# Kernel tuning notes

Measured on AMD Instinct MI355X. Metric: run time of the kernel, lower is better.

## Reference

```python
import jax, jax.numpy as jnp
import numpy as np

B, N, D, H, W, C = 2, 4, 48, 28, 60, 64
DOWNSAMPLE = 8
NX, NY, NZ = 192, 192, 1   # from size=(192,192), scale=0.25; zbound=[-10,10,20] -> nz=1
SCALE = 0.25
OFFSETX = 0
DMIN, DMAX, DSTEP = 2.0, 50.0, 1.0


def setup_inputs() -> dict:
    key = jax.random.key(0)
    x = jax.random.normal(key, (B, N, D, H, W, C), dtype=jnp.float32)
    ogfW, ogfH = W * DOWNSAMPLE, H * DOWNSAMPLE
    fx = fy = 250.0
    K = jnp.array([[fx, 0.0, ogfW / 2.0], [0.0, fy, ogfH / 2.0], [0.0, 0.0, 1.0]], jnp.float32)
    intrinsics = jnp.broadcast_to(K, (B, N, 3, 3))
    # camera->ego rotation: cam z (forward) -> ego x, cam x (right) -> ego -y, cam y (down) -> ego -z
    R = jnp.array([[0.0, 0.0, 1.0], [-1.0, 0.0, 0.0], [0.0, -1.0, 0.0]], jnp.float32)
    pose = jnp.zeros((B, N, 4, 4), jnp.float32)
    pose = pose.at[..., :3, :3].set(R)
    pose = pose.at[..., :3, 3].set(jnp.array([1.0, 0.0, 1.6], jnp.float32))
    pose = pose.at[..., 3, 3].set(1.0)
    return {"x": x, "intrinsics": intrinsics, "pose": pose}


def _frustum():
    # (D,H,W,3) frustum of (u*d, v*d, d) homogeneous pixel coords scaled by depth
    ds = jnp.arange(DMIN, DMAX, DSTEP, dtype=jnp.float32)          # (D,)
    xs = jnp.linspace(0.0, W * DOWNSAMPLE - 1, W, dtype=jnp.float32)
    ys = jnp.linspace(0.0, H * DOWNSAMPLE - 1, H, dtype=jnp.float32)
    d = jnp.broadcast_to(ds[:, None, None], (D, H, W))
    u = jnp.broadcast_to(xs[None, None, :], (D, H, W))
    v = jnp.broadcast_to(ys[None, :, None], (D, H, W))
    return jnp.stack([u * d, v * d, d], axis=-1)


def reference(x, intrinsics, pose):
    rots = pose[..., :3, :3]                 # (B,N,3,3)
    trans = pose[..., :3, 3]                 # (B,N,3)
    pts = _frustum()                         # (D,H,W,3)
    combine = rots @ jnp.linalg.inv(intrinsics)  # (B,N,3,3)
    # ego-frame point cloud: (B,N,D,H,W,3)
    geom = jnp.einsum('bnij,dhwj->bndhwi', combine, pts) + trans[:, :, None, None, None, :]
    # bev_intrinsics from bev_params_to_intrinsics(size, scale, offsetx)
    f_bev = 1.0 / SCALE
    cx_bev = NX / 2.0 + OFFSETX
    cy_bev = NY / 2.0
    # torch .long() truncates toward zero, same as astype(int32)
    gx = (geom[..., 0] * f_bev + cx_bev).astype(jnp.int32)
    gy = (geom[..., 1] * f_bev + cy_bev).astype(jnp.int32)
    gz = ((geom[..., 2] + 10.0) / 20.0).astype(jnp.int32)  # (z - bx2 + dx2/2)/dx2, bx2=0, dx2=20
    b = jnp.broadcast_to(jnp.arange(B, dtype=jnp.int32)[:, None, None, None, None], gx.shape)
    kept = (gx >= 0) & (gx < NX) & (gy >= 0) & (gy < NY) & (gz >= 0) & (gz < NZ)
    # segment scatter-add == sort + cumsum-diff + scatter-set (ranks unique after reduction)
    flat = ((b * NZ + gz) * NY + gy) * NX + gx
    flat = jnp.where(kept, flat, 0).reshape(-1)
    xf = jnp.where(kept[..., None], x, jnp.zeros((), x.dtype)).reshape(-1, C)
    out = jnp.zeros((B * NZ * NY * NX, C), x.dtype).at[flat].add(xf)
    out = out.reshape(B, NZ, NY, NX, C)
    # final[b, :, z, y, x] layout then cat(unbind(dim=2), dim=1) -> (B, NZ*C, NY, NX)
    return out.transpose(0, 1, 4, 2, 3).reshape(B, NZ * C, NY, NX)
```

## Files before the change

### kernel.cpp

```cpp
#include <hip/hip_runtime.h>

#define BB 2
#define NN 4
#define DD 48
#define HH 28
#define WW 60
#define CC 64
#define NXg 192
#define NYg 192
#define NZg 1
#define DOWNS 8

constexpr int PTS    = BB * NN * DD * HH * WW;
constexpr int NCELLS = BB * NZg * NYg * NXg;
constexpr int CH_STRIDE = NYg * NXg;
constexpr int CHUNK = 64;
constexpr int MAXWORK = NCELLS + PTS / CHUNK + 64;
constexpr int NBLK = NCELLS / 1024;

__global__ void __launch_bounds__(256)
geom_hist_kernel(const float* __restrict__ intr,
                 const float* __restrict__ pose,
                 int* __restrict__ sidx,
                 int* __restrict__ rankv,
                 int* __restrict__ counts) {
    __shared__ int hkey[512];
    __shared__ int hval[512];
    __shared__ int hbase[512];

    int tid = threadIdx.x;
    for (int s = tid; s < 512; s += 256) { hkey[s] = -1; hval[s] = 0; }
    __syncthreads();

    int p = blockIdx.x * blockDim.x + tid;
    int w = p % WW;
    int t = p / WW;
    int h = t % HH; t /= HH;
    int d = t % DD; t /= DD;
    int n = t % NN;
    int b = t / NN;

    const float* K  = intr + (size_t)(b * NN + n) * 9;
    const float* Pm = pose + (size_t)(b * NN + n) * 16;

    double k00 = K[0], k01 = K[1], k02 = K[2];
    double k10 = K[3], k11 = K[4], k12 = K[5];
    double k20 = K[6], k21 = K[7], k22 = K[8];

    double det = k00 * (k11 * k22 - k12 * k21)
               - k01 * (k10 * k22 - k12 * k20)
               + k02 * (k10 * k21 - k11 * k20);
    double id = 1.0 / det;
    double i00 = (k11 * k22 - k12 * k21) * id;
    double i01 = (k02 * k21 - k01 * k22) * id;
    double i02 = (k01 * k12 - k02 * k11) * id;
    double i10 = (k12 * k20 - k10 * k22) * id;
    double i11 = (k00 * k22 - k02 * k20) * id;
    double i12 = (k02 * k10 - k00 * k12) * id;
    double i20 = (k10 * k21 - k11 * k20) * id;
    double i21 = (k01 * k20 - k00 * k21) * id;
    double i22 = (k00 * k11 - k01 * k10) * id;

    double r00 = Pm[0],  r01 = Pm[1],  r02 = Pm[2],  tx = Pm[3];
    double r10 = Pm[4],  r11 = Pm[5],  r12 = Pm[6],  ty = Pm[7];
    double r20 = Pm[8],  r21 = Pm[9],  r22 = Pm[10], tz = Pm[11];

    double c00 = r00 * i00 + r01 * i10 + r02 * i20;
    double c01 = r00 * i01 + r01 * i11 + r02 * i21;
    double c02 = r00 * i02 + r01 * i12 + r02 * i22;
    double c10 = r10 * i00 + r11 * i10 + r12 * i20;
    double c11 = r10 * i01 + r11 * i11 + r12 * i21;
    double c12 = r10 * i02 + r11 * i12 + r12 * i22;
    double c20 = r20 * i00 + r21 * i10 + r22 * i20;
    double c21 = r20 * i01 + r21 * i11 + r22 * i21;
    double c22 = r20 * i02 + r21 * i12 + r22 * i22;

    double u   = (double)w * ((double)(WW * DOWNS - 1) / (double)(WW - 1));
    double v   = (double)h * ((double)(HH * DOWNS - 1) / (double)(HH - 1));
    double dep = 2.0 + (double)d;
    double px = u * dep, py = v * dep, pz = dep;

    double gxf = (c00 * px + c01 * py + c02 * pz + tx) * 4.0 + 96.0;
    double gyf = (c10 * px + c11 * py + c12 * pz + ty) * 4.0 + 96.0;
    double gzf = ((c20 * px + c21 * py + c22 * pz + tz) + 10.0) / 20.0;

    int gx = (int)gxf;
    int gy = (int)gyf;
    int gz = (int)gzf;

    bool kept = (gx >= 0) & (gx < NXg) & (gy >= 0) & (gy < NYg) &
                (gz >= 0) & (gz < NZg);

    int cell = kept ? (((b * NZg + gz) * NYg + gy) * NXg + gx) : -1;
    sidx[p] = cell;

    int slot = -1, lrank = 0;
    if (cell >= 0) {
        unsigned hsh = ((unsigned)cell * 2654435761u) >> 21;
        slot = (int)(hsh & 511u);
        while (true) {
            int prev = atomicCAS(&hkey[slot], -1, cell);
            if (prev == -1 || prev == cell) break;
            slot = (slot + 1) & 511;
        }
        lrank = atomicAdd(&hval[slot], 1);
    }
    __syncthreads();
    for (int s = tid; s < 512; s += 256) {
        int k = hkey[s];
        if (k >= 0) hbase[s] = atomicAdd(&counts[k], hval[s]);
    }
    __syncthreads();
    if (cell >= 0) rankv[p] = hbase[slot] + lrank;
}

__global__ void __launch_bounds__(1024)
blocksum_kernel(const int* __restrict__ counts,
                long long* __restrict__ blocksum) {
    __shared__ long long wsum[16];
    int tid = threadIdx.x, lane = tid & 63, wv = tid >> 6;
    int cell = blockIdx.x * 1024 + tid;
    int cnt = counts[cell];
    long long packed = ((long long)cnt << 24) | (long long)((cnt + 63) >> 6);
    #pragma unroll
    for (int o = 32; o > 0; o >>= 1) packed += __shfl_down(packed, o, 64);
    if (lane == 0) wsum[wv] = packed;
    __syncthreads();
    if (tid == 0) {
        long long s = 0;
        #pragma unroll
        for (int k = 0; k < 16; ++k) s += wsum[k];
        blocksum[blockIdx.x] = s;
    }
}

__global__ void __launch_bounds__(1024)
scan_emit_kernel(const int* __restrict__ counts,
                 const long long* __restrict__ blocksum,
                 int* __restrict__ offsets,
                 int* __restrict__ worklist,
                 int* __restrict__ nwork) {
    __shared__ long long wsum[16];
    __shared__ long long base_sh;
    int tid = threadIdx.x, lane = tid & 63, wv = tid >> 6;

    if (tid == 0) {
        long long s = 0;
        int nb = blockIdx.x;
        for (int j = 0; j < nb; ++j) s += blocksum[j];
        base_sh = s;
    }

    int cell = blockIdx.x * 1024 + tid;
    int cnt  = counts[cell];
    int nch  = (cnt + 63) >> 6;
    long long packed = ((long long)cnt << 24) | (long long)nch;

    long long incl = packed;
    #pragma unroll
    for (int o = 1; o < 64; o <<= 1) {
        long long tt = __shfl_up(incl, o, 64);
        if (lane >= o) incl += tt;
    }
    if (lane == 63) wsum[wv] = incl;
    __syncthreads();
    if (tid == 0) {
        long long run = 0;
        #pragma unroll
        for (int k = 0; k < 16; ++k) { long long tt = wsum[k]; wsum[k] = run; run += tt; }
    }
    __syncthreads();

    long long excl = base_sh + wsum[wv] + incl - packed;
    int off   = (int)(excl >> 24);
    int wbase = (int)(excl & 0xFFFFFF);

    offsets[cell] = off;
    for (int c = 0; c < nch; ++c) worklist[wbase + c] = (cell << 14) | c;
    if (blockIdx.x == NBLK - 1 && tid == 1023) *nwork = wbase + nch;
}

__global__ void fill_kernel(const int* __restrict__ sidx,
                            const int* __restrict__ rankv,
                            const int* __restrict__ offsets,
                            int* __restrict__ bins) {
    int p = blockIdx.x * blockDim.x + threadIdx.x;
    if (p >= PTS) return;
    int cell = sidx[p];
    if (cell < 0) return;
    bins[offsets[cell] + rankv[p]] = p;
}

__global__ void __launch_bounds__(256)
gather_kernel(const float* __restrict__ x,
              const int* __restrict__ counts,
              const int* __restrict__ offsets,
              const int* __restrict__ bins,
              const int* __restrict__ worklist,
              const int* __restrict__ nwork,
              float* __restrict__ out) {
    int lane = threadIdx.x & 63;
    int gw   = blockIdx.x * (blockDim.x >> 6) + (threadIdx.x >> 6);
    int stride = gridDim.x * (blockDim.x >> 6);
    int n = *nwork;

    for (int j = gw; j < n; j += stride) {
        int e    = worklist[j];
        int cell = e >> 14;
        int ch   = e & 16383;
        int off  = offsets[cell] + (ch << 6);
        int m    = counts[cell] - (ch << 6);
        if (m > CHUNK) m = CHUNK;

        int bid = (lane < m) ? bins[off + lane] : 0;

        float a0 = 0.f, a1 = 0.f, a2 = 0.f, a3 = 0.f;
        float a4 = 0.f, a5 = 0.f, a6 = 0.f, a7 = 0.f;
        int i = 0;
        for (; i + 8 <= m; i += 8) {
            int p0 = __shfl(bid, i + 0);
            int p1 = __shfl(bid, i + 1);
            int p2 = __shfl(bid, i + 2);
            int p3 = __shfl(bid, i + 3);
            int p4 = __shfl(bid, i + 4);
            int p5 = __shfl(bid, i + 5);
            int p6 = __shfl(bid, i + 6);
            int p7 = __shfl(bid, i + 7);
            a0 += x[(size_t)p0 * CC + lane];
            a1 += x[(size_t)p1 * CC + lane];
            a2 += x[(size_t)p2 * CC + lane];
            a3 += x[(size_t)p3 * CC + lane];
            a4 += x[(size_t)p4 * CC + lane];
            a5 += x[(size_t)p5 * CC + lane];
            a6 += x[(size_t)p6 * CC + lane];
            a7 += x[(size_t)p7 * CC + lane];
        }
        for (; i < m; ++i) {
            int p0 = __shfl(bid, i);
            a0 += x[(size_t)p0 * CC + lane];
        }
        float s = ((a0 + a1) + (a2 + a3)) + ((a4 + a5) + (a6 + a7));

        int yx = cell % (NYg * NXg);
        int bz = cell / (NYg * NXg);
        atomicAdd(&out[((size_t)bz * CC + lane) * CH_STRIDE + yx], s);
    }
}

extern "C" void kernel_launch(void* const* d_in, const int* in_sizes, int n_in,
                              void* d_out, int out_size, void* d_ws, size_t ws_size,
                              hipStream_t stream) {
    const float* x    = (const float*)d_in[0];
    const float* intr = (const float*)d_in[1];
    const float* pose = (const float*)d_in[2];
    float* out = (float*)d_out;

    int* sidx       = (int*)d_ws;
    int* rankv      = sidx + PTS;
    int* counts     = rankv + PTS;
    int* offsets    = counts + NCELLS;
    long long* bsum = (long long*)(offsets + NCELLS);
    int* worklist   = (int*)(bsum + NBLK);
    int* nwork      = worklist + MAXWORK;
    int* bins       = nwork + 1;

    hipMemsetAsync(out, 0, (size_t)out_size * sizeof(float), stream);
    hipMemsetAsync(counts, 0, (size_t)NCELLS * sizeof(int), stream);

    geom_hist_kernel<<<PTS / 256, 256, 0, stream>>>(intr, pose, sidx, rankv, counts);
    blocksum_kernel<<<NBLK, 1024, 0, stream>>>(counts, bsum);
    scan_emit_kernel<<<NBLK, 1024, 0, stream>>>(counts, bsum, offsets, worklist, nwork);
    fill_kernel<<<(PTS + 255) / 256, 256, 0, stream>>>(sidx, rankv, offsets, bins);
    gather_kernel<<<1024, 256, 0, stream>>>(x, counts, offsets, bins, worklist, nwork, out);
}
```

Before: 256.9 us.

## Replace sort-based binning with wavefront-local run-merged atomic scatter plus transpose

Drops the histogram, scan, fill and gather pipeline. Each wavefront now walks its valid points, merges consecutive points that fall in the same cell, and atomically adds 64-channel rows into a channel-last scratch buffer. A tiled shared-memory transpose then writes the channel-first output. This removes four kernel launches and the index bookkeeping traffic, but relies on neighbouring points mapping to the same cell to keep global float atomic contention low.

Result: slower. 276.3 us (+7.5%).

```diff
diff --git a/kernel.cpp b/kernel.cpp
--- a/kernel.cpp
+++ b/kernel.cpp
@@ -13,26 +13,17 @@
 
 constexpr int PTS    = BB * NN * DD * HH * WW;
 constexpr int NCELLS = BB * NZg * NYg * NXg;
-constexpr int CH_STRIDE = NYg * NXg;
-constexpr int CHUNK = 64;
-constexpr int MAXWORK = NCELLS + PTS / CHUNK + 64;
-constexpr int NBLK = NCELLS / 1024;
+constexpr int NYX    = NYg * NXg;
 
 __global__ void __launch_bounds__(256)
-geom_hist_kernel(const float* __restrict__ intr,
-                 const float* __restrict__ pose,
-                 int* __restrict__ sidx,
-                 int* __restrict__ rankv,
-                 int* __restrict__ counts) {
-    __shared__ int hkey[512];
-    __shared__ int hval[512];
-    __shared__ int hbase[512];
+scatter_kernel(const float* __restrict__ x,
+               const float* __restrict__ intr,
+               const float* __restrict__ pose,
+               float* __restrict__ outT) {
+    int tid  = threadIdx.x;
+    int lane = tid & 63;
+    int p    = blockIdx.x * 256 + tid;
 
-    int tid = threadIdx.x;
-    for (int s = tid; s < 512; s += 256) { hkey[s] = -1; hval[s] = 0; }
-    __syncthreads();
-
-    int p = blockIdx.x * blockDim.x + tid;
     int w = p % WW;
     int t = p / WW;
     int h = t % HH; t /= HH;
@@ -92,158 +83,52 @@
                 (gz >= 0) & (gz < NZg);
 
     int cell = kept ? (((b * NZg + gz) * NYg + gy) * NXg + gx) : -1;
-    sidx[p] = cell;
 
-    int slot = -1, lrank = 0;
-    if (cell >= 0) {
-        unsigned hsh = ((unsigned)cell * 2654435761u) >> 21;
-        slot = (int)(hsh & 511u);
-        while (true) {
-            int prev = atomicCAS(&hkey[slot], -1, cell);
-            if (prev == -1 || prev == cell) break;
-            slot = (slot + 1) & 511;
+    unsigned long long mask = __ballot(cell >= 0);
+    if (mask == 0ULL) return;
+
+    int base = p - lane;
+    float acc = 0.f;
+    int   cur = -1;
+    while (mask) {
+        int ks = __ffsll((long long)mask) - 1;
+        mask &= mask - 1ULL;
+        int ck = __shfl(cell, ks);
+        float xv = x[(size_t)(base + ks) * CC + lane];
+        if (ck != cur) {
+            if (cur >= 0) atomicAdd(&outT[(size_t)cur * CC + lane], acc);
+            cur = ck;
+            acc = 0.f;
         }
-        lrank = atomicAdd(&hval[slot], 1);
+        acc += xv;
     }
-    __syncthreads();
-    for (int s = tid; s < 512; s += 256) {
-        int k = hkey[s];
-        if (k >= 0) hbase[s] = atomicAdd(&counts[k], hval[s]);
-    }
-    __syncthreads();
-    if (cell >= 0) rankv[p] = hbase[slot] + lrank;
+    atomicAdd(&outT[(size_t)cur * CC + lane], acc);
 }
 
-__global__ void __launch_bounds__(1024)
-blocksum_kernel(const int* __restrict__ counts,
-                long long* __restrict__ blocksum) {
-    __shared__ long long wsum[16];
-    int tid = threadIdx.x, lane = tid & 63, wv = tid >> 6;
-    int cell = blockIdx.x * 1024 + tid;
-    int cnt = counts[cell];
-    long long packed = ((long long)cnt << 24) | (long long)((cnt + 63) >> 6);
+__global__ void __launch_bounds__(256)
+transpose_kernel(const float* __restrict__ outT,
+                 float* __restrict__ out) {
+    __shared__ float tile[64][65];
+    int tid      = threadIdx.x;
+    int cellbase = blockIdx.x * 64;
+
+    const float* src = outT + (size_t)cellbase * CC;
     #pragma unroll
-    for (int o = 32; o > 0; o >>= 1) packed += __shfl_down(packed, o, 64);
-    if (lane == 0) wsum[wv] = packed;
-    __syncthreads();
-    if (tid == 0) {
-        long long s = 0;
-        #pragma unroll
-        for (int k = 0; k < 16; ++k) s += wsum[k];
-        blocksum[blockIdx.x] = s;
-    }
-}
-
-__global__ void __launch_bounds__(1024)
-scan_emit_kernel(const int* __restrict__ counts,
-                 const long long* __restrict__ blocksum,
-                 int* __restrict__ offsets,
-                 int* __restrict__ worklist,
-                 int* __restrict__ nwork) {
-    __shared__ long long wsum[16];
-    __shared__ long long base_sh;
-    int tid = threadIdx.x, lane = tid & 63, wv = tid >> 6;
-
-    if (tid == 0) {
-        long long s = 0;
-        int nb = blockIdx.x;
-        for (int j = 0; j < nb; ++j) s += blocksum[j];
-        base_sh = s;
-    }
-
-    int cell = blockIdx.x * 1024 + tid;
-    int cnt  = counts[cell];
-    int nch  = (cnt + 63) >> 6;
-    long long packed = ((long long)cnt << 24) | (long long)nch;
-
-    long long incl = packed;
-    #pragma unroll
-    for (int o = 1; o < 64; o <<= 1) {
-        long long tt = __shfl_up(incl, o, 64);
-        if (lane >= o) incl += tt;
-    }
-    if (lane == 63) wsum[wv] = incl;
-    __syncthreads();
-    if (tid == 0) {
-        long long run = 0;
-        #pragma unroll
-        for (int k = 0; k < 16; ++k) { long long tt = wsum[k]; wsum[k] = run; run += tt; }
+    for (int i = 0; i < 16; ++i) {
+        int idx = i * 256 + tid;
+        tile[idx >> 6][idx & 63] = src[idx];
     }
     __syncthreads();
 
-    long long excl = base_sh + wsum[wv] + incl - packed;
-    int off   = (int)(excl >> 24);
-    int wbase = (int)(excl & 0xFFFFFF);
-
-    offsets[cell] = off;
-    for (int c = 0; c < nch; ++c) worklist[wbase + c] = (cell << 14) | c;
-    if (blockIdx.x == NBLK - 1 && tid == 1023) *nwork = wbase + nch;
-}
-
-__global__ void fill_kernel(const int* __restrict__ sidx,
-                            const int* __restrict__ rankv,
-                            const int* __restrict__ offsets,
-                            int* __restrict__ bins) {
-    int p = blockIdx.x * blockDim.x + threadIdx.x;
-    if (p >= PTS) return;
-    int cell = sidx[p];
-    if (cell < 0) return;
-    bins[offsets[cell] + rankv[p]] = p;
-}
-
-__global__ void __launch_bounds__(256)
-gather_kernel(const float* __restrict__ x,
-              const int* __restrict__ counts,
-              const int* __restrict__ offsets,
-              const int* __restrict__ bins,
-              const int* __restrict__ worklist,
-              const int* __restrict__ nwork,
-              float* __restrict__ out) {
-    int lane = threadIdx.x & 63;
-    int gw   = blockIdx.x * (blockDim.x >> 6) + (threadIdx.x >> 6);
-    int stride = gridDim.x * (blockDim.x >> 6);
-    int n = *nwork;
-
-    for (int j = gw; j < n; j += stride) {
-        int e    = worklist[j];
-        int cell = e >> 14;
-        int ch   = e & 16383;
-        int off  = offsets[cell] + (ch << 6);
-        int m    = counts[cell] - (ch << 6);
-        if (m > CHUNK) m = CHUNK;
-
-        int bid = (lane < m) ? bins[off + lane] : 0;
-
-        float a0 = 0.f, a1 = 0.f, a2 = 0.f, a3 = 0.f;
-        float a4 = 0.f, a5 = 0.f, a6 = 0.f, a7 = 0.f;
-        int i = 0;
-        for (; i + 8 <= m; i += 8) {
-            int p0 = __shfl(bid, i + 0);
-            int p1 = __shfl(bid, i + 1);
-            int p2 = __shfl(bid, i + 2);
-            int p3 = __shfl(bid, i + 3);
-            int p4 = __shfl(bid, i + 4);
-            int p5 = __shfl(bid, i + 5);
-            int p6 = __shfl(bid, i + 6);
-            int p7 = __shfl(bid, i + 7);
-            a0 += x[(size_t)p0 * CC + lane];
-            a1 += x[(size_t)p1 * CC + lane];
-            a2 += x[(size_t)p2 * CC + lane];
-            a3 += x[(size_t)p3 * CC + lane];
-            a4 += x[(size_t)p4 * CC + lane];
-            a5 += x[(size_t)p5 * CC + lane];
-            a6 += x[(size_t)p6 * CC + lane];
-            a7 += x[(size_t)p7 * CC + lane];
-        }
-        for (; i < m; ++i) {
-            int p0 = __shfl(bid, i);
-            a0 += x[(size_t)p0 * CC + lane];
-        }
-        float s = ((a0 + a1) + (a2 + a3)) + ((a4 + a5) + (a6 + a7));
-
-        int yx = cell % (NYg * NXg);
-        int bz = cell / (NYg * NXg);
-        atomicAdd(&out[((size_t)bz * CC + lane) * CH_STRIDE + yx], s);
+    int bb     = cellbase / NYX;
+    int yxbase = cellbase % NYX;
+    float* dst = out + (size_t)bb * CC * NYX + yxbase;
+    #pragma unroll
+    for (int i = 0; i < 16; ++i) {
+        int idx = i * 256 + tid;
+        int ch  = idx >> 6;
+        int cl  = idx & 63;
+        dst[(size_t)ch * NYX + cl] = tile[cl][ch];
     }
 }
 
@@ -255,21 +140,9 @@
     const float* pose = (const float*)d_in[2];
     float* out = (float*)d_out;
 
-    int* sidx       = (int*)d_ws;
-    int* rankv      = sidx + PTS;
-    int* counts     = rankv + PTS;
-    int* offsets    = counts + NCELLS;
-    long long* bsum = (long long*)(offsets + NCELLS);
-    int* worklist   = (int*)(bsum + NBLK);
-    int* nwork      = worklist + MAXWORK;
-    int* bins       = nwork + 1;
+    float* outT = (float*)d_ws;
 
-    hipMemsetAsync(out, 0, (size_t)out_size * sizeof(float), stream);
-    hipMemsetAsync(counts, 0, (size_t)NCELLS * sizeof(int), stream);
-
-    geom_hist_kernel<<<PTS / 256, 256, 0, stream>>>(intr, pose, sidx, rankv, counts);
-    blocksum_kernel<<<NBLK, 1024, 0, stream>>>(counts, bsum);
-    scan_emit_kernel<<<NBLK, 1024, 0, stream>>>(counts, bsum, offsets, worklist, nwork);
-    fill_kernel<<<(PTS + 255) / 256, 256, 0, stream>>>(sidx, rankv, offsets, bins);
-    gather_kernel<<<1024, 256, 0, stream>>>(x, counts, offsets, bins, worklist, nwork, out);
+    hipMemsetAsync(outT, 0, (size_t)NCELLS * CC * sizeof(float), stream);
+    scatter_kernel<<<PTS / 256, 256, 0, stream>>>(x, intr, pose, outT);
+    transpose_kernel<<<NCELLS / 64, 256, 0, stream>>>(outT, out);
 }
```
